# Kernel optimization log

Measured on AMD Instinct MI355X. Metric: run time of the kernel, lower is better.

Reference implementation:

```python
import jax, jax.numpy as jnp
import numpy as np

IM_H, IM_W = 32, 32
HEADS, HEAD_DIM = 8, 32
IN_DIM = 256
OUT_DIM = 256
N = IM_H * IM_W


def _relative_indices(h, w):
    # replicate torch meshgrid('ij') + flatten logic
    gy, gx = np.meshgrid(np.arange(h), np.arange(w), indexing='ij')
    pos = np.stack([gy.reshape(-1), gx.reshape(-1)])  # (2, n)
    rel = pos[:, :, None] - pos[:, None, :]           # (2, n, n)
    r0 = (rel[0] + (h - 1)) * (2 * w - 1)
    r1 = rel[1] + (w - 1)
    return (r0 + r1).reshape(-1)                      # (n*n,)

_REL_IDX = jnp.asarray(_relative_indices(IM_H, IM_W), dtype=jnp.int32)


def setup_inputs() -> dict:
    key = jax.random.key(0)
    ks = jax.random.split(key, 8)
    d_inner = HEADS * HEAD_DIM
    x = jax.random.normal(ks[0], (16, N, IN_DIM), dtype=jnp.float32)
    Wq = jax.random.normal(ks[1], (IN_DIM, d_inner), dtype=jnp.float32) / np.sqrt(IN_DIM)
    Wk = jax.random.normal(ks[2], (IN_DIM, d_inner), dtype=jnp.float32) / np.sqrt(IN_DIM)
    Wv = jax.random.normal(ks[3], (IN_DIM, d_inner), dtype=jnp.float32) / np.sqrt(IN_DIM)
    bias_table = jax.random.normal(ks[4], ((2 * IM_H - 1) * (2 * IM_W - 1), HEADS), dtype=jnp.float32)
    Wo = jax.random.normal(ks[5], (d_inner, OUT_DIM), dtype=jnp.float32) / np.sqrt(d_inner)
    bo = jax.random.normal(ks[6], (OUT_DIM,), dtype=jnp.float32) * 0.01
    return {"x": x, "Wq": Wq, "Wk": Wk, "Wv": Wv, "bias_table": bias_table, "Wo": Wo, "bo": bo}


def reference(x, Wq, Wk, Wv, bias_table, Wo, bo):
    b, n, _ = x.shape
    scale = HEAD_DIM ** (-0.5)
    # QKV projections -> [b, h, n, d]
    def proj(W):
        return (x @ W).reshape(b, n, HEADS, HEAD_DIM).transpose(0, 2, 1, 3)
    Q, K, V = proj(Wq), proj(Wk), proj(Wv)
    # gathered relative position bias -> [1, h, n, n]
    bias = bias_table[_REL_IDX].reshape(n, n, HEADS).transpose(2, 0, 1)[None]
    scores = jnp.einsum('bhnd,bhmd->bhnm', Q, K) * scale + bias
    attn = jax.nn.softmax(scores, axis=-1)
    out = jnp.einsum('bhnm,bhmd->bhnd', attn, V)
    out = out.transpose(0, 2, 1, 3).reshape(b, n, HEADS * HEAD_DIM)
    return out @ Wo + bo  # dropout is identity in eval mode
```

## Files before the change

kernel.cpp:

```cpp
#include <hip/hip_runtime.h>


using f32x4  = __attribute__((ext_vector_type(4))) float;
using bf16x8 = __attribute__((ext_vector_type(8))) short;

__device__ __forceinline__ short f2bf(float f) {
  union { float f; unsigned u; } v; v.f = f;
  return (short)((v.u + 0x7FFFu + ((v.u >> 16) & 1u)) >> 16);
}
__device__ __forceinline__ f32x4 mfma_k32(bf16x8 a, bf16x8 b, f32x4 c) {
  return __builtin_amdgcn_mfma_f32_16x16x32_bf16(a, b, c, 0, 0, 0);
}
__device__ __forceinline__ int cvt_pk_bf16(float lo, float hi) {
  int r;
  asm("v_cvt_pk_bf16_f32 %0, %1, %2" : "=v"(r) : "v"(lo), "v"(hi));
  return r;
}
__device__ __forceinline__ f32x4 ldb(const float* __restrict__ row, int p) {
  f32x4 v;
  v[0] = row[p]; v[1] = row[p - 1]; v[2] = row[p - 2]; v[3] = row[p - 3];
  return v;
}

#define CSQ 0.25500526817f

__global__ __launch_bounds__(256) void k_prep(const float* __restrict__ Wq,
    const float* __restrict__ Wk, const float* __restrict__ Wv,
    const float* __restrict__ Wo, short* __restrict__ WT,
    const float* __restrict__ bt, float* __restrict__ Tg) {
  int bx = blockIdx.x;
  if (bx < 64) {
    __shared__ float tile[64][65];
    int wid = bx >> 4, t = bx & 15;
    int ro0 = (t & 3) * 64, co0 = (t >> 2) * 64;
    const float* W = wid == 0 ? Wq : wid == 1 ? Wk : wid == 2 ? Wv : Wo;
    int tr = threadIdx.x >> 4, tc = threadIdx.x & 15;
    #pragma unroll
    for (int c = 0; c < 4; ++c) {
      int row = c * 16 + tr;
      float4 v = *reinterpret_cast<const float4*>(
          &W[(ro0 + row) * 256 + co0 + tc * 4]);
      tile[row][tc * 4 + 0] = v.x;
      tile[row][tc * 4 + 1] = v.y;
      tile[row][tc * 4 + 2] = v.z;
      tile[row][tc * 4 + 3] = v.w;
    }
    __syncthreads();
    #pragma unroll
    for (int c = 0; c < 4; ++c) {
      int orow = c * 16 + tr;
      short4 s;
      s.x = f2bf(tile[tc * 4 + 0][orow]);
      s.y = f2bf(tile[tc * 4 + 1][orow]);
      s.z = f2bf(tile[tc * 4 + 2][orow]);
      s.w = f2bf(tile[tc * 4 + 3][orow]);
      *reinterpret_cast<short4*>(
          &WT[wid * 65536 + (co0 + orow) * 256 + ro0 + tc * 4]) = s;
    }
  } else {
    int idx = (bx - 64) * 256 + threadIdx.x;
    int h = idx >> 12, i = idx & 4095;
    if (i < 3969) Tg[idx] = bt[i * 8 + h] * 1.4426950408889634f;
  }
}

__global__ __launch_bounds__(256) void k_qkv(const float* __restrict__ x,
    const short* __restrict__ WT,
    short* __restrict__ Q, short* __restrict__ K, short* __restrict__ Vt) {
  __shared__ short Wlds[2][4096];
  char* lbase = (char*)Wlds;
  const int tid = threadIdx.x;
  const int w = tid >> 6, l = tid & 63, lr = l & 15, lg = l >> 4;
  const int m0 = blockIdx.x * 64;
  const int wi = blockIdx.y;
  const char* Wb = (const char*)(WT + wi * 65536);
  const float* xrow = x + (size_t)(m0 + w * 16 + lr) * 256;
  bf16x8 af[8];
  #pragma unroll
  for (int kc = 0; kc < 8; ++kc) {
    float4 a = *reinterpret_cast<const float4*>(xrow + kc * 32 + lg * 8);
    float4 c = *reinterpret_cast<const float4*>(xrow + kc * 32 + lg * 8 + 4);
    union { int i4[4]; bf16x8 v; } u;
    u.i4[0] = cvt_pk_bf16(a.x, a.y);
    u.i4[1] = cvt_pk_bf16(a.z, a.w);
    u.i4[2] = cvt_pk_bf16(c.x, c.y);
    u.i4[3] = cvt_pk_bf16(c.z, c.w);
    af[kc] = u.v;
  }
  const int Lb0 = tid * 16, Lb1 = 4096 + tid * 16;
  const int P0 = Lb0 ^ (((Lb0 >> 9) & 7) << 4);
  const int P1 = Lb1 ^ (((Lb1 >> 9) & 7) << 4);
  int rdo[8];
  #pragma unroll
  for (int kc = 0; kc < 8; ++kc) {
    int Lg = lr * 512 + kc * 64 + lg * 16;
    rdo[kc] = Lg ^ ((lr & 7) << 4);
  }
  {
    int4 s0 = *reinterpret_cast<const int4*>(Wb + Lb0);
    int4 s1 = *reinterpret_cast<const int4*>(Wb + Lb1);
    *reinterpret_cast<int4*>(lbase + P0) = s0;
    *reinterpret_cast<int4*>(lbase + P1) = s1;
  }
  __syncthreads();
  #pragma unroll 2
  for (int nt = 0; nt < 16; ++nt) {
    const int cur = nt & 1, nxt = cur ^ 1;
    int4 t0, t1;
    if (nt < 15) {
      t0 = *reinterpret_cast<const int4*>(Wb + (nt + 1) * 8192 + Lb0);
      t1 = *reinterpret_cast<const int4*>(Wb + (nt + 1) * 8192 + Lb1);
    }
    f32x4 acc = {0.f, 0.f, 0.f, 0.f};
    #pragma unroll
    for (int kc = 0; kc < 8; ++kc) {
      bf16x8 bfr = *reinterpret_cast<const bf16x8*>(lbase + cur * 8192 + rdo[kc]);
      acc = mfma_k32(af[kc], bfr, acc);
    }
    int colb = nt * 16 + lr;
    int h = colb >> 5, d = colb & 31;
    if (wi == 2) {
      int m = m0 + w * 16 + lg * 4;
      int b = m >> 10, n0 = m & 1023;
      int js = n0 >> 5;
      int lgv = (n0 & 15) >> 2, hi = (n0 >> 4) & 1;
      int jp = lgv * 8 + hi * 4;
      short4 vv;
      vv.x = f2bf(acc[0]); vv.y = f2bf(acc[1]);
      vv.z = f2bf(acc[2]); vv.w = f2bf(acc[3]);
      *reinterpret_cast<short4*>(
          &Vt[(((size_t)(b * 8 + h) * 32 + js) << 10) + d * 32 + jp]) = vv;
    } else {
      #pragma unroll
      for (int r = 0; r < 4; ++r) {
        int m = m0 + w * 16 + lg * 4 + r;
        int b = m >> 10, n = m & 1023;
        short val = (wi == 0) ? f2bf(acc[r] * CSQ) : f2bf(acc[r]);
        if (wi == 0)
          Q[((size_t)(b * 8 + h) * 1024 + n) * 32 + d] = val;
        else
          K[((size_t)(b * 8 + h) * 1024 + n) * 32 + d] = val;
      }
    }
    if (nt < 15) {
      *reinterpret_cast<int4*>(lbase + nxt * 8192 + P0) = t0;
      *reinterpret_cast<int4*>(lbase + nxt * 8192 + P1) = t1;
    }
    __syncthreads();
  }
}

__global__ __launch_bounds__(512) void k_attn(const short* __restrict__ Q,
    const short* __restrict__ K, const short* __restrict__ Vt,
    const float* __restrict__ Tg, short* __restrict__ aout) {
  __shared__ char smraw[24576];
  float* Tlds = (float*)smraw;
  auto mO  = (float(*)[4][4][64])smraw;
  auto mls = (float(*)[2][4][64])(smraw + 16384);
  const int tid = threadIdx.x, bid = blockIdx.x;
  const int h = bid & 7, qt = (bid >> 3) & 7, b = bid >> 6;
  const float* Th = Tg + (h << 12);
  for (int t = tid; t < 3969; t += 512) Tlds[t] = Th[t];
  __syncthreads();
  const int wg = tid >> 6, l = tid & 63, lr = l & 15, lg = l >> 4;
  const int w = wg & 3, jh = wg >> 2;
  const size_t hoff = (size_t)(b * 8 + h) << 15;
  const short* Qh = Q + hoff;
  const short* Kh = K + hoff;
  const short* Vh = Vt + hoff;
  const int ita = qt * 4 + w;
  const int i0a = ita * 16;
  const int i0b = i0a + 512;
  const int yia = ita >> 1;
  const int pbase = ((ita & 1) << 4) + lr - lg * 4 + 31;
  bf16x8 qfa = *reinterpret_cast<const bf16x8*>(&Qh[(i0a + lr) * 32 + lg * 8]);
  bf16x8 qfb = *reinterpret_cast<const bf16x8*>(&Qh[(i0b + lr) * 32 + lg * 8]);
  bf16x8 ones;
  #pragma unroll
  for (int e = 0; e < 8; ++e) ones[e] = (short)0x3F80;
  f32x4 oa0 = {0.f,0.f,0.f,0.f}, oa1 = {0.f,0.f,0.f,0.f};
  f32x4 ob0 = {0.f,0.f,0.f,0.f}, ob1 = {0.f,0.f,0.f,0.f};
  f32x4 lsa = {0.f,0.f,0.f,0.f}, lsb = {0.f,0.f,0.f,0.f};
  const int koff0 = lr * 32 + lg * 8, koff1 = (16 + lr) * 32 + lg * 8;
  const int js0 = jh * 16, jsE = js0 + 16;
  const float* Trow0 = &Tlds[(yia - js0 + 31) * 63];
  bf16x8 kf0 = *reinterpret_cast<const bf16x8*>(&Kh[(js0 << 10) + koff0]);
  bf16x8 kf1 = *reinterpret_cast<const bf16x8*>(&Kh[(js0 << 10) + koff1]);
  bf16x8 vf0 = *reinterpret_cast<const bf16x8*>(&Vh[(js0 << 10) + koff0]);
  bf16x8 vf1 = *reinterpret_cast<const bf16x8*>(&Vh[(js0 << 10) + koff1]);
  f32x4 bA0 = ldb(Trow0, pbase);
  f32x4 bA1 = ldb(Trow0, pbase - 16);
  f32x4 bB0 = ldb(Trow0 + 1008, pbase);
  f32x4 bB1 = ldb(Trow0 + 1008, pbase - 16);
  #pragma unroll 4
  for (int t = 0; t < 16; ++t) {
    const int js = js0 + t;
    const int jn = (js + 1 < jsE) ? js + 1 : js;
    bf16x8 nkf0 = *reinterpret_cast<const bf16x8*>(&Kh[(jn << 10) + koff0]);
    bf16x8 nkf1 = *reinterpret_cast<const bf16x8*>(&Kh[(jn << 10) + koff1]);
    bf16x8 nvf0 = *reinterpret_cast<const bf16x8*>(&Vh[(jn << 10) + koff0]);
    bf16x8 nvf1 = *reinterpret_cast<const bf16x8*>(&Vh[(jn << 10) + koff1]);
    const int tn = (t + 1 < 16) ? t + 1 : 15;
    const float* TrowN = Trow0 - tn * 63;
    f32x4 nbA0 = ldb(TrowN, pbase);
    f32x4 nbA1 = ldb(TrowN, pbase - 16);
    f32x4 nbB0 = ldb(TrowN + 1008, pbase);
    f32x4 nbB1 = ldb(TrowN + 1008, pbase - 16);
    f32x4 sa0 = mfma_k32(kf0, qfa, bA0);
    f32x4 sa1 = mfma_k32(kf1, qfa, bA1);
    f32x4 sb0 = mfma_k32(kf0, qfb, bB0);
    f32x4 sb1 = mfma_k32(kf1, qfb, bB1);
    float pa0[4], pa1[4], pb0[4], pb1[4];
    #pragma unroll
    for (int r = 0; r < 4; ++r) {
      pa0[r] = __builtin_amdgcn_exp2f(sa0[r]);
      pa1[r] = __builtin_amdgcn_exp2f(sa1[r]);
      pb0[r] = __builtin_amdgcn_exp2f(sb0[r]);
      pb1[r] = __builtin_amdgcn_exp2f(sb1[r]);
    }
    union { int i4[4]; bf16x8 v; } pka, pkb;
    pka.i4[0] = cvt_pk_bf16(pa0[0], pa0[1]);
    pka.i4[1] = cvt_pk_bf16(pa0[2], pa0[3]);
    pka.i4[2] = cvt_pk_bf16(pa1[0], pa1[1]);
    pka.i4[3] = cvt_pk_bf16(pa1[2], pa1[3]);
    pkb.i4[0] = cvt_pk_bf16(pb0[0], pb0[1]);
    pkb.i4[1] = cvt_pk_bf16(pb0[2], pb0[3]);
    pkb.i4[2] = cvt_pk_bf16(pb1[0], pb1[1]);
    pkb.i4[3] = cvt_pk_bf16(pb1[2], pb1[3]);
    oa0 = mfma_k32(pka.v, vf0, oa0);
    oa1 = mfma_k32(pka.v, vf1, oa1);
    lsa = mfma_k32(pka.v, ones, lsa);
    ob0 = mfma_k32(pkb.v, vf0, ob0);
    ob1 = mfma_k32(pkb.v, vf1, ob1);
    lsb = mfma_k32(pkb.v, ones, lsb);
    kf0 = nkf0; kf1 = nkf1; vf0 = nvf0; vf1 = nvf1;
    bA0 = nbA0; bA1 = nbA1; bB0 = nbB0; bB1 = nbB1;
  }
  __syncthreads();
  if (jh == 1) {
    #pragma unroll
    for (int r = 0; r < 4; ++r) {
      mO[w][0][r][l] = oa0[r];
      mO[w][1][r][l] = oa1[r];
      mO[w][2][r][l] = ob0[r];
      mO[w][3][r][l] = ob1[r];
      mls[w][0][r][l] = lsa[r];
      mls[w][1][r][l] = lsb[r];
    }
  }
  __syncthreads();
  if (jh == 0) {
    #pragma unroll
    for (int r = 0; r < 4; ++r) {
      oa0[r] += mO[w][0][r][l];
      oa1[r] += mO[w][1][r][l];
      ob0[r] += mO[w][2][r][l];
      ob1[r] += mO[w][3][r][l];
      lsa[r] += mls[w][0][r][l];
      lsb[r] += mls[w][1][r][l];
    }
    #pragma unroll
    for (int r = 0; r < 4; ++r) {
      float invr = 1.0f / lsa[r];
      int n = i0a + lg * 4 + r;
      size_t base = ((size_t)b << 18) + (size_t)n * 256 + h * 32;
      aout[base + lr]      = f2bf(oa0[r] * invr);
      aout[base + 16 + lr] = f2bf(oa1[r] * invr);
    }
    #pragma unroll
    for (int r = 0; r < 4; ++r) {
      float invr = 1.0f / lsb[r];
      int n = i0b + lg * 4 + r;
      size_t base = ((size_t)b << 18) + (size_t)n * 256 + h * 32;
      aout[base + lr]      = f2bf(ob0[r] * invr);
      aout[base + 16 + lr] = f2bf(ob1[r] * invr);
    }
  }
}

__global__ __launch_bounds__(256) void k_outproj(const short* __restrict__ aout,
    const short* __restrict__ WoT, const float* __restrict__ bo,
    float* __restrict__ out) {
  __shared__ short Wlds[2][4096];
  char* lbase = (char*)Wlds;
  const int tid = threadIdx.x;
  const int w = tid >> 6, l = tid & 63, lr = l & 15, lg = l >> 4;
  const int m0 = blockIdx.x * 64;
  const int nt0 = blockIdx.y * 8;
  const char* Wb = (const char*)WoT + nt0 * 8192;
  const short* arow = aout + (size_t)(m0 + w * 16 + lr) * 256;
  bf16x8 af[8];
  #pragma unroll
  for (int kc = 0; kc < 8; ++kc)
    af[kc] = *reinterpret_cast<const bf16x8*>(arow + kc * 32 + lg * 8);
  const int Lb0 = tid * 16, Lb1 = 4096 + tid * 16;
  const int P0 = Lb0 ^ (((Lb0 >> 9) & 7) << 4);
  const int P1 = Lb1 ^ (((Lb1 >> 9) & 7) << 4);
  int rdo[8];
  #pragma unroll
  for (int kc = 0; kc < 8; ++kc) {
    int Lg = lr * 512 + kc * 64 + lg * 16;
    rdo[kc] = Lg ^ ((lr & 7) << 4);
  }
  {
    int4 s0 = *reinterpret_cast<const int4*>(Wb + Lb0);
    int4 s1 = *reinterpret_cast<const int4*>(Wb + Lb1);
    *reinterpret_cast<int4*>(lbase + P0) = s0;
    *reinterpret_cast<int4*>(lbase + P1) = s1;
  }
  __syncthreads();
  #pragma unroll 2
  for (int t = 0; t < 8; ++t) {
    const int cur = t & 1, nxt = cur ^ 1;
    int4 t0, t1;
    if (t < 7) {
      t0 = *reinterpret_cast<const int4*>(Wb + (t + 1) * 8192 + Lb0);
      t1 = *reinterpret_cast<const int4*>(Wb + (t + 1) * 8192 + Lb1);
    }
    f32x4 acc = {0.f, 0.f, 0.f, 0.f};
    #pragma unroll
    for (int kc = 0; kc < 8; ++kc) {
      bf16x8 bfr = *reinterpret_cast<const bf16x8*>(lbase + cur * 8192 + rdo[kc]);
      acc = mfma_k32(af[kc], bfr, acc);
    }
    int colb = (nt0 + t) * 16 + lr;
    float bias = bo[colb];
    #pragma unroll
    for (int r = 0; r < 4; ++r) {
      int m = m0 + w * 16 + lg * 4 + r;
      out[(size_t)m * 256 + colb] = acc[r] + bias;
    }
    if (t < 7) {
      *reinterpret_cast<int4*>(lbase + nxt * 8192 + P0) = t0;
      *reinterpret_cast<int4*>(lbase + nxt * 8192 + P1) = t1;
    }
    __syncthreads();
  }
}

extern "C" void kernel_launch(void* const* d_in, const int* in_sizes, int n_in,
                              void* d_out, int out_size, void* d_ws, size_t ws_size,
                              hipStream_t stream) {
  const float* x  = (const float*)d_in[0];
  const float* Wq = (const float*)d_in[1];
  const float* Wk = (const float*)d_in[2];
  const float* Wv = (const float*)d_in[3];
  const float* bt = (const float*)d_in[4];
  const float* Wo = (const float*)d_in[5];
  const float* bo = (const float*)d_in[6];
  float* out = (float*)d_out;
  char* ws = (char*)d_ws;
  short* WT   = (short*)ws;
  short* Qs   = (short*)(ws + 512 * 1024);
  short* Ks   = Qs + 4194304;
  short* Vts  = Ks + 4194304;
  short* aout = Vts + 4194304;
  float* Tg   = (float*)(ws + 512 * 1024 + 4ull * 8388608);

  k_prep<<<192, 256, 0, stream>>>(Wq, Wk, Wv, Wo, WT, bt, Tg);
  k_qkv<<<dim3(256, 3), 256, 0, stream>>>(x, WT, Qs, Ks, Vts);
  k_attn<<<1024, 512, 0, stream>>>(Qs, Ks, Vts, Tg, aout);
  k_outproj<<<dim3(256, 2), 256, 0, stream>>>(aout, WT + 3 * 65536, bo, out);
}
```

Measured before the change: 76.57 us.

## Load weight tiles directly into LDS with global_load_lds and pre-swizzled layout

Weight tiles in the QKV and output-projection GEMMs are now loaded with direct global-to-LDS loads instead of going through registers and separate LDS stores. To keep the bank-conflict-avoiding swizzle, the prep kernel now writes the transposed weights already XOR-swizzled in global memory, so the linear LDS copy reproduces the old layout. This removes register staging and the LDS store instructions. The trade-off is that correctness now depends on the swizzle matching the read offsets and on the asynchronous load being complete at the barrier.

```diff
diff --git a/kernel.cpp b/kernel.cpp
--- a/kernel.cpp
+++ b/kernel.cpp
@@ -20,6 +20,11 @@
   f32x4 v;
   v[0] = row[p]; v[1] = row[p - 1]; v[2] = row[p - 2]; v[3] = row[p - 3];
   return v;
+}
+__device__ __forceinline__ void gload16(const void* g, void* l) {
+  __builtin_amdgcn_global_load_lds(
+      (__attribute__((address_space(1))) const unsigned int*)g,
+      (__attribute__((address_space(3))) unsigned int*)l, 16, 0, 0);
 }
 
 #define CSQ 0.25500526817f
@@ -49,13 +54,14 @@
     #pragma unroll
     for (int c = 0; c < 4; ++c) {
       int orow = c * 16 + tr;
+      int n = co0 + orow, k = ro0 + tc * 4;
       short4 s;
       s.x = f2bf(tile[tc * 4 + 0][orow]);
       s.y = f2bf(tile[tc * 4 + 1][orow]);
       s.z = f2bf(tile[tc * 4 + 2][orow]);
       s.w = f2bf(tile[tc * 4 + 3][orow]);
-      *reinterpret_cast<short4*>(
-          &WT[wid * 65536 + (co0 + orow) * 256 + ro0 + tc * 4]) = s;
+      int so = (n * 256 + k) ^ ((n & 7) << 3);
+      *reinterpret_cast<short4*>(&WT[wid * 65536 + so]) = s;
     }
   } else {
     int idx = (bx - 64) * 256 + threadIdx.x;
@@ -87,29 +93,23 @@
     u.i4[3] = cvt_pk_bf16(c.z, c.w);
     af[kc] = u.v;
   }
-  const int Lb0 = tid * 16, Lb1 = 4096 + tid * 16;
-  const int P0 = Lb0 ^ (((Lb0 >> 9) & 7) << 4);
-  const int P1 = Lb1 ^ (((Lb1 >> 9) & 7) << 4);
   int rdo[8];
   #pragma unroll
   for (int kc = 0; kc < 8; ++kc) {
     int Lg = lr * 512 + kc * 64 + lg * 16;
     rdo[kc] = Lg ^ ((lr & 7) << 4);
   }
-  {
-    int4 s0 = *reinterpret_cast<const int4*>(Wb + Lb0);
-    int4 s1 = *reinterpret_cast<const int4*>(Wb + Lb1);
-    *reinterpret_cast<int4*>(lbase + P0) = s0;
-    *reinterpret_cast<int4*>(lbase + P1) = s1;
-  }
+  const int wb = w << 10;
+  const int gofs = tid * 16;
+  gload16(Wb + gofs,        lbase + wb);
+  gload16(Wb + 4096 + gofs, lbase + 4096 + wb);
   __syncthreads();
   #pragma unroll 2
   for (int nt = 0; nt < 16; ++nt) {
     const int cur = nt & 1, nxt = cur ^ 1;
-    int4 t0, t1;
     if (nt < 15) {
-      t0 = *reinterpret_cast<const int4*>(Wb + (nt + 1) * 8192 + Lb0);
-      t1 = *reinterpret_cast<const int4*>(Wb + (nt + 1) * 8192 + Lb1);
+      gload16(Wb + (nt + 1) * 8192 + gofs,        lbase + nxt * 8192 + wb);
+      gload16(Wb + (nt + 1) * 8192 + 4096 + gofs, lbase + nxt * 8192 + 4096 + wb);
     }
     f32x4 acc = {0.f, 0.f, 0.f, 0.f};
     #pragma unroll
@@ -141,10 +141,6 @@
         else
           K[((size_t)(b * 8 + h) * 1024 + n) * 32 + d] = val;
       }
-    }
-    if (nt < 15) {
-      *reinterpret_cast<int4*>(lbase + nxt * 8192 + P0) = t0;
-      *reinterpret_cast<int4*>(lbase + nxt * 8192 + P1) = t1;
     }
     __syncthreads();
   }
@@ -293,29 +289,23 @@
   #pragma unroll
   for (int kc = 0; kc < 8; ++kc)
     af[kc] = *reinterpret_cast<const bf16x8*>(arow + kc * 32 + lg * 8);
-  const int Lb0 = tid * 16, Lb1 = 4096 + tid * 16;
-  const int P0 = Lb0 ^ (((Lb0 >> 9) & 7) << 4);
-  const int P1 = Lb1 ^ (((Lb1 >> 9) & 7) << 4);
   int rdo[8];
   #pragma unroll
   for (int kc = 0; kc < 8; ++kc) {
     int Lg = lr * 512 + kc * 64 + lg * 16;
     rdo[kc] = Lg ^ ((lr & 7) << 4);
   }
-  {
-    int4 s0 = *reinterpret_cast<const int4*>(Wb + Lb0);
-    int4 s1 = *reinterpret_cast<const int4*>(Wb + Lb1);
-    *reinterpret_cast<int4*>(lbase + P0) = s0;
-    *reinterpret_cast<int4*>(lbase + P1) = s1;
-  }
+  const int wb = w << 10;
+  const int gofs = tid * 16;
+  gload16(Wb + gofs,        lbase + wb);
+  gload16(Wb + 4096 + gofs, lbase + 4096 + wb);
   __syncthreads();
   #pragma unroll 2
   for (int t = 0; t < 8; ++t) {
     const int cur = t & 1, nxt = cur ^ 1;
-    int4 t0, t1;
     if (t < 7) {
-      t0 = *reinterpret_cast<const int4*>(Wb + (t + 1) * 8192 + Lb0);
-      t1 = *reinterpret_cast<const int4*>(Wb + (t + 1) * 8192 + Lb1);
+      gload16(Wb + (t + 1) * 8192 + gofs,        lbase + nxt * 8192 + wb);
+      gload16(Wb + (t + 1) * 8192 + 4096 + gofs, lbase + nxt * 8192 + 4096 + wb);
     }
     f32x4 acc = {0.f, 0.f, 0.f, 0.f};
     #pragma unroll
@@ -329,10 +319,6 @@
     for (int r = 0; r < 4; ++r) {
       int m = m0 + w * 16 + lg * 4 + r;
       out[(size_t)m * 256 + colb] = acc[r] + bias;
-    }
-    if (t < 7) {
-      *reinterpret_cast<int4*>(lbase + nxt * 8192 + P0) = t0;
-      *reinterpret_cast<int4*>(lbase + nxt * 8192 + P1) = t1;
     }
     __syncthreads();
   }
```

Result: no change. 77.55 us (+1.3%).
